# Kernel tuning notes

Hardware: AMD Instinct MI355X
Metric: run time of the kernel (lower is better)

Reference implementation:

```python
import jax, jax.numpy as jnp
import numpy as np

N_NODES = 50000
N_EDGES = 800000
FEATS = 128
HIDDEN = 64
CLASSES = 64


def graph_conv(x, edges):
    """GCN-style symmetric-normalized aggregation over an edge list (no self-loops;
    self information is supplied via the concat in the host module)."""
    src, dst = edges[0], edges[1]
    ones = jnp.ones((edges.shape[1],), dtype=x.dtype)
    deg = jax.ops.segment_sum(ones, dst, num_segments=N_NODES)
    inv_sqrt = jax.lax.rsqrt(jnp.maximum(deg, 1.0))
    coef = inv_sqrt[src] * inv_sqrt[dst]            # [E]
    msg = x[src] * coef[:, None]                     # [E, H] gather
    return jax.ops.segment_sum(msg, dst, num_segments=N_NODES)  # [N, H] scatter


def setup_inputs() -> dict:
    key = jax.random.key(0)
    ks = jax.random.split(key, 16)
    def lin(k, out_d, in_d):
        return jax.random.normal(k, (out_d, in_d), dtype=jnp.float32) / np.sqrt(in_d)
    x = jax.random.normal(ks[0], (N_NODES, FEATS), dtype=jnp.float32)
    edges = jax.random.randint(ks[1], (2, N_EDGES), 0, N_NODES, dtype=jnp.int64)
    return {
        "x": x,
        "edges": edges,
        "W1": lin(ks[2], HIDDEN, FEATS),
        "b1": jnp.zeros((HIDDEN,), dtype=jnp.float32),
        "W2": lin(ks[3], HIDDEN, 2 * HIDDEN),
        "A2a": lin(ks[4], HIDDEN, HIDDEN),
        "A2b": lin(ks[5], HIDDEN, HIDDEN),
        "W3": lin(ks[6], HIDDEN, 2 * HIDDEN),
        "A3a": lin(ks[7], HIDDEN, HIDDEN),
        "A3b": lin(ks[8], HIDDEN, HIDDEN),
        "W4": lin(ks[9], CLASSES, 2 * HIDDEN),
        "A4a": lin(ks[10], CLASSES, HIDDEN),
        "A4b": lin(ks[11], CLASSES, HIDDEN),
    }


def _block(x, edges, W, Aa, Ab):
    # relu(Linear(cat[x, conv(x)]) + att_a(x) * att_b(x))
    h = graph_conv(x, edges)
    cat = jnp.concatenate([x, h], axis=1)            # [N, 2H]
    return jax.nn.relu(cat @ W.T + (x @ Aa.T) * (x @ Ab.T))


def reference(x, edges, W1, b1, W2, A2a, A2b, W3, A3a, A3b, W4, A4a, A4b):
    x = jax.nn.relu(x @ W1.T + b1)                   # [N, H]
    x = _block(x, edges, W2, A2a, A2b)               # [N, H]
    x = _block(x, edges, W3, A3a, A3b)               # [N, H]
    x = _block(x, edges, W4, A4a, A4b)               # [N, C]
    return x
```

## Files before the change

kernel.cpp:

```cpp
#include <hip/hip_runtime.h>
#include <hip/hip_bf16.h>
#include <hip/hip_fp16.h>

#define N_NODES 50000
#define N_EDGES 800000
#define NTILES 3125
#define W_TOTAL 57344
#define WB2 192
#define TB 782
#define ROWCAP 64
#define ZROW N_NODES

#define NBKT 200
#define BKT_NODES 250
#define BKT_CAP 4400
#define ABLK 256
#define ACH ((N_EDGES + ABLK - 1) / ABLK)

typedef __attribute__((ext_vector_type(8))) short bf16x8;
typedef __attribute__((ext_vector_type(4))) float f32x4;
typedef __attribute__((ext_vector_type(2))) float f32x2;
typedef __attribute__((ext_vector_type(8))) unsigned short u16x8;
typedef __attribute__((ext_vector_type(4))) unsigned int u32x4;

__device__ inline unsigned short f2bf(float f) {
    unsigned int x = __float_as_uint(f);
    unsigned int r = (x + 0x7FFF + ((x >> 16) & 1)) >> 16;
    return (unsigned short)r;
}
__device__ inline float2 h2f2(unsigned int u) {
    __half2 h = *(__half2*)&u;
    return make_float2(__low2float(h), __high2float(h));
}
__device__ inline unsigned int f22h2(float a, float b) {
    __half2 h = __floats2half2_rn(a, b);
    return *(unsigned int*)&h;
}

__global__ __launch_bounds__(256) void passA_kernel(
    const float* __restrict__ x, const int* __restrict__ src, const int* __restrict__ dst,
    const float* __restrict__ W1, const float* __restrict__ b1,
    const float* W2, const float* A2a, const float* A2b,
    const float* W3, const float* A3a, const float* A3b,
    const float* W4, const float* A4a, const float* A4b,
    int* __restrict__ bucketCnt, unsigned int* __restrict__ bktArr,
    unsigned short* __restrict__ wp, __half* __restrict__ Ht,
    unsigned char* __restrict__ As8, unsigned char* __restrict__ Bs8) {
    int tid = threadIdx.x;

    if (blockIdx.x < ABLK) {
        __shared__ int hist[NBKT];
        __shared__ int gbase[NBKT];
        __shared__ int hoff[NBKT];
        if (tid < NBKT) { hist[tid] = 0; hoff[tid] = 0; }
        __syncthreads();
        int e0 = blockIdx.x * ACH;
        int e1 = min(e0 + ACH, N_EDGES);
        for (int e = e0 + tid; e < e1; e += 256)
            atomicAdd(&hist[dst[e] / BKT_NODES], 1);
        __syncthreads();
        if (tid < NBKT) {
            int h = hist[tid];
            gbase[tid] = h ? atomicAdd(&bucketCnt[tid], h) : 0;
        }
        __syncthreads();
        for (int e = e0 + tid; e < e1; e += 256) {
            int d = dst[e];
            int b = d / BKT_NODES;
            int pos = gbase[b] + atomicAdd(&hoff[b], 1);
            if (pos < BKT_CAP)
                bktArr[(size_t)b * BKT_CAP + pos] =
                    ((unsigned int)(d - b * BKT_NODES) << 16) | (unsigned int)src[e];
        }
        return;
    }
    if (blockIdx.x >= ABLK + TB) {
        if (blockIdx.x == ABLK + TB) {
            if (tid < 16)      ((unsigned int*)(As8 + (size_t)ZROW * 64))[tid] = 0u;
            else if (tid < 32) ((unsigned int*)(Bs8 + (size_t)ZROW * 64))[tid - 16] = 0u;
        }
        int i = 8192 + (blockIdx.x - ABLK - TB) * 256 + tid;
        if (i >= W_TOTAL) return;
        float v;
        if (i < 16384)      v = W2[i - 8192];
        else if (i < 20480) v = A2a[i - 16384];
        else if (i < 24576) v = A2b[i - 20480];
        else if (i < 32768) v = W3[i - 24576];
        else if (i < 36864) v = A3a[i - 32768];
        else if (i < 40960) v = A3b[i - 36864];
        else if (i < 49152) v = W4[i - 40960];
        else if (i < 53248) v = A4a[i - 49152];
        else                v = A4b[i - 53248];
        wp[i] = f2bf(v);
        return;
    }

    int wave = ((blockIdx.x - ABLK) * 256 + tid) >> 6;
    if (wave >= NTILES) return;
    int lane = tid & 63;
    int r16 = lane & 15, quad = lane >> 4;
    int base = wave * 16;

    bf16x8 a[4];
    const float* xr = x + (size_t)(base + r16) * 128 + quad * 8;
#pragma unroll
    for (int kb = 0; kb < 4; kb++) {
        float4 f0 = *(const float4*)(xr + kb * 32);
        float4 f1 = *(const float4*)(xr + kb * 32 + 4);
        bf16x8 v;
        v[0] = (short)f2bf(f0.x); v[1] = (short)f2bf(f0.y);
        v[2] = (short)f2bf(f0.z); v[3] = (short)f2bf(f0.w);
        v[4] = (short)f2bf(f1.x); v[5] = (short)f2bf(f1.y);
        v[6] = (short)f2bf(f1.z); v[7] = (short)f2bf(f1.w);
        a[kb] = v;
    }

#pragma unroll
    for (int jt = 0; jt < 4; jt++) {
        f32x4 acc = {0.f, 0.f, 0.f, 0.f};
        const float* wr = W1 + (size_t)(jt * 16 + r16) * 128 + quad * 8;
#pragma unroll
        for (int kb = 0; kb < 4; kb++) {
            float4 g0 = *(const float4*)(wr + kb * 32);
            float4 g1 = *(const float4*)(wr + kb * 32 + 4);
            bf16x8 b;
            b[0] = (short)f2bf(g0.x); b[1] = (short)f2bf(g0.y);
            b[2] = (short)f2bf(g0.z); b[3] = (short)f2bf(g0.w);
            b[4] = (short)f2bf(g1.x); b[5] = (short)f2bf(g1.y);
            b[6] = (short)f2bf(g1.z); b[7] = (short)f2bf(g1.w);
            acc = __builtin_amdgcn_mfma_f32_16x16x32_bf16(a[kb], b, acc, 0, 0, 0);
        }
        int col = jt * 16 + r16;
        float bias = b1[col];
#pragma unroll
        for (int r = 0; r < 4; r++) {
            int row = base + quad * 4 + r;
            float v = fmaxf(acc[r] + bias, 0.f);
            Ht[(size_t)row * 64 + col] = __float2half(v);
        }
    }
}

__global__ __launch_bounds__(256) void csr_scale_k(const int* __restrict__ bucketCnt,
                                                   const unsigned int* __restrict__ bktArr,
                                                   const __half* __restrict__ Ht,
                                                   unsigned short* __restrict__ srcAp,
                                                   int* __restrict__ cnt,
                                                   __half* __restrict__ As,
                                                   unsigned char* __restrict__ As8,
                                                   float* __restrict__ isq,
                                                   float* __restrict__ sdeg) {
    __shared__ int lcnt[BKT_NODES];
    int b = blockIdx.x, tid = threadIdx.x;
    if (tid < BKT_NODES) lcnt[tid] = 0;
    __syncthreads();
    int n = min(bucketCnt[b], BKT_CAP);
    int rowbase = b * BKT_NODES;
    const unsigned int* arr = bktArr + (size_t)b * BKT_CAP;
    for (int i = tid; i < n; i += 256) {
        unsigned int u = arr[i];
        int dl = (int)(u >> 16);
        int pos = atomicAdd(&lcnt[dl], 1);
        if (pos < ROWCAP)
            srcAp[(size_t)(rowbase + dl) * ROWCAP + pos] = (unsigned short)(u & 0xFFFF);
    }
    __syncthreads();
    if (tid < BKT_NODES) {
        int deg = lcnt[tid];
        int cv = min(deg, ROWCAP);
        int cvr = (cv + 7) & ~7;
        for (int j = cv; j < cvr; j++)
            srcAp[(size_t)(rowbase + tid) * ROWCAP + j] = (unsigned short)ZROW;
        cnt[rowbase + tid] = deg;
        float dv = fmaxf((float)deg, 1.0f);
        isq[rowbase + tid] = rsqrtf(dv);
        sdeg[rowbase + tid] = sqrtf(dv);
    }
    __syncthreads();
    int sl = tid & 15;
    for (int rr = tid >> 4; rr < BKT_NODES; rr += 16) {
        int row = rowbase + rr;
        float is = rsqrtf(fmaxf((float)lcnt[rr], 1.0f));
        uint2 rv = *((const uint2*)(Ht + (size_t)row * 64) + sl);
        float2 fa = h2f2(rv.x), fb = h2f2(rv.y);
        float s0 = fa.x * is, s1 = fa.y * is, s2 = fb.x * is, s3 = fb.y * is;
        uint2 ov;
        ov.x = f22h2(s0, s1);
        ov.y = f22h2(s2, s3);
        *((uint2*)(As + (size_t)row * 64) + sl) = ov;
        unsigned int w = __builtin_amdgcn_cvt_pk_fp8_f32(s0, s1, 0, false);
        w = __builtin_amdgcn_cvt_pk_fp8_f32(s2, s3, w, true);
        ((unsigned int*)As8)[(size_t)row * 16 + sl] = w;
    }
}

__global__ __launch_bounds__(256) void conv_dense_k(const __half* __restrict__ hs,
                                                    const unsigned char* __restrict__ hs8,
                                                    const int* __restrict__ cnt,
                                                    const unsigned short* __restrict__ srcAp,
                                                    const float* __restrict__ isq,
                                                    const float* __restrict__ sdeg,
                                                    const unsigned short* __restrict__ wp,
                                                    const unsigned short* __restrict__ aap,
                                                    const unsigned short* __restrict__ abp,
                                                    __half* __restrict__ outs,
                                                    unsigned char* __restrict__ outs8,
                                                    float* __restrict__ outf,
                                                    int finalLayer) {
    __shared__ unsigned short clds[64][64];
    int tid = threadIdx.x;
    int wv = tid >> 6;
    int lane = tid & 63;
    int t = blockIdx.x * 4 + wv;
    if (t >= NTILES) return;
    int base = t * 16;

    {
        int r = lane >> 2, fl = lane & 3;
        int row = base + r;
        int b = row * ROWCAP;
        int cv = min(cnt[row], ROWCAP);
        int cvr = (cv + 7) & ~7;
        f32x2 acc[8];
#pragma unroll
        for (int k = 0; k < 8; k++) acc[k] = (f32x2){0.f, 0.f};
        if (cvr) {
            u16x8 sv = __builtin_nontemporal_load((const u16x8*)(srcAp + b));
            for (int i = 0; i < cvr; i += 8) {
                u16x8 svn = sv;
                if (i + 8 < cvr)
                    svn = __builtin_nontemporal_load((const u16x8*)(srcAp + b + i + 8));
                u32x4 rv[8];
#pragma unroll
                for (int u = 0; u < 8; u++)
                    rv[u] = *((const u32x4*)(hs8 + (size_t)(int)sv[u] * 64) + fl);
#pragma unroll
                for (int u = 0; u < 8; u++) {
                    acc[0] += __builtin_amdgcn_cvt_pk_f32_fp8(rv[u][0], false);
                    acc[1] += __builtin_amdgcn_cvt_pk_f32_fp8(rv[u][0], true);
                    acc[2] += __builtin_amdgcn_cvt_pk_f32_fp8(rv[u][1], false);
                    acc[3] += __builtin_amdgcn_cvt_pk_f32_fp8(rv[u][1], true);
                    acc[4] += __builtin_amdgcn_cvt_pk_f32_fp8(rv[u][2], false);
                    acc[5] += __builtin_amdgcn_cvt_pk_f32_fp8(rv[u][2], true);
                    acc[6] += __builtin_amdgcn_cvt_pk_f32_fp8(rv[u][3], false);
                    acc[7] += __builtin_amdgcn_cvt_pk_f32_fp8(rv[u][3], true);
                }
                sv = svn;
            }
        }
        float sc = isq[row];
        u16x8 o0, o1;
#pragma unroll
        for (int k = 0; k < 4; k++) {
            o0[2 * k]     = f2bf(acc[k][0] * sc);
            o0[2 * k + 1] = f2bf(acc[k][1] * sc);
            o1[2 * k]     = f2bf(acc[4 + k][0] * sc);
            o1[2 * k + 1] = f2bf(acc[4 + k][1] * sc);
        }
        *(u16x8*)(&clds[wv * 16 + r][fl * 16]) = o0;
        *(u16x8*)(&clds[wv * 16 + r][fl * 16 + 8]) = o1;
    }

    int r16 = lane & 15, quad = lane >> 4;
    float rs = sdeg[base + r16];
    const u32x4* hp = (const u32x4*)(hs + (size_t)(base + r16) * 64);
    u32x4 raw0 = __builtin_nontemporal_load(hp + quad);
    u32x4 raw1 = __builtin_nontemporal_load(hp + 4 + quad);
    bf16x8 ha0, ha1;
    {
        float2 f;
        f = h2f2(raw0[0]); ha0[0] = (short)f2bf(f.x * rs); ha0[1] = (short)f2bf(f.y * rs);
        f = h2f2(raw0[1]); ha0[2] = (short)f2bf(f.x * rs); ha0[3] = (short)f2bf(f.y * rs);
        f = h2f2(raw0[2]); ha0[4] = (short)f2bf(f.x * rs); ha0[5] = (short)f2bf(f.y * rs);
        f = h2f2(raw0[3]); ha0[6] = (short)f2bf(f.x * rs); ha0[7] = (short)f2bf(f.y * rs);
        f = h2f2(raw1[0]); ha1[0] = (short)f2bf(f.x * rs); ha1[1] = (short)f2bf(f.y * rs);
        f = h2f2(raw1[1]); ha1[2] = (short)f2bf(f.x * rs); ha1[3] = (short)f2bf(f.y * rs);
        f = h2f2(raw1[2]); ha1[4] = (short)f2bf(f.x * rs); ha1[5] = (short)f2bf(f.y * rs);
        f = h2f2(raw1[3]); ha1[6] = (short)f2bf(f.x * rs); ha1[7] = (short)f2bf(f.y * rs);
    }
    bf16x8 ca0 = *(const bf16x8*)(&clds[wv * 16 + r16][quad * 8]);
    bf16x8 ca1 = *(const bf16x8*)(&clds[wv * 16 + r16][32 + quad * 8]);

    float isq4[4];
    if (!finalLayer) {
#pragma unroll
        for (int r = 0; r < 4; r++) isq4[r] = isq[base + quad * 4 + r];
    }

#pragma unroll
    for (int jt = 0; jt < 4; jt++) {
        const unsigned short* wr = wp + (size_t)(jt * 16 + r16) * 128 + quad * 8;
        const unsigned short* ar = aap + (size_t)(jt * 16 + r16) * 64 + quad * 8;
        const unsigned short* br = abp + (size_t)(jt * 16 + r16) * 64 + quad * 8;
        f32x4 P = {0.f, 0.f, 0.f, 0.f};
        f32x4 Q = {0.f, 0.f, 0.f, 0.f};
        f32x4 R = {0.f, 0.f, 0.f, 0.f};
        P = __builtin_amdgcn_mfma_f32_16x16x32_bf16(ha0, *(const bf16x8*)(wr), P, 0, 0, 0);
        P = __builtin_amdgcn_mfma_f32_16x16x32_bf16(ha1, *(const bf16x8*)(wr + 32), P, 0, 0, 0);
        P = __builtin_amdgcn_mfma_f32_16x16x32_bf16(ca0, *(const bf16x8*)(wr + 64), P, 0, 0, 0);
        P = __builtin_amdgcn_mfma_f32_16x16x32_bf16(ca1, *(const bf16x8*)(wr + 96), P, 0, 0, 0);
        Q = __builtin_amdgcn_mfma_f32_16x16x32_bf16(ha0, *(const bf16x8*)(ar), Q, 0, 0, 0);
        Q = __builtin_amdgcn_mfma_f32_16x16x32_bf16(ha1, *(const bf16x8*)(ar + 32), Q, 0, 0, 0);
        R = __builtin_amdgcn_mfma_f32_16x16x32_bf16(ha0, *(const bf16x8*)(br), R, 0, 0, 0);
        R = __builtin_amdgcn_mfma_f32_16x16x32_bf16(ha1, *(const bf16x8*)(br + 32), R, 0, 0, 0);
        int col = jt * 16 + r16;
#pragma unroll
        for (int r = 0; r < 4; r++) {
            int row = base + quad * 4 + r;
            float v = fmaxf(P[r] + Q[r] * R[r], 0.f);
            if (finalLayer) {
                __builtin_nontemporal_store(v, &outf[(size_t)row * 64 + col]);
            } else {
                float vs = v * isq4[r];
                __half hv = __float2half(vs);
                __builtin_nontemporal_store(*(unsigned short*)&hv,
                                            (unsigned short*)outs + (size_t)row * 64 + col);
                unsigned int pb = __builtin_amdgcn_cvt_pk_fp8_f32(vs, vs, 0, false);
                __builtin_nontemporal_store((unsigned char)pb,
                                            &outs8[(size_t)row * 64 + col]);
            }
        }
    }
}

extern "C" void kernel_launch(void* const* d_in, const int* in_sizes, int n_in,
                              void* d_out, int out_size, void* d_ws, size_t ws_size,
                              hipStream_t stream) {
    const float* x = (const float*)d_in[0];
    const int* edges = (const int*)d_in[1];
    const float* W1 = (const float*)d_in[2];
    const float* b1 = (const float*)d_in[3];
    const float* W2 = (const float*)d_in[4];
    const float* A2a = (const float*)d_in[5];
    const float* A2b = (const float*)d_in[6];
    const float* W3 = (const float*)d_in[7];
    const float* A3a = (const float*)d_in[8];
    const float* A3b = (const float*)d_in[9];
    const float* W4 = (const float*)d_in[10];
    const float* A4a = (const float*)d_in[11];
    const float* A4b = (const float*)d_in[12];
    float* out = (float*)d_out;

    const int* src = edges;
    const int* dst = edges + N_EDGES;

    char* p = (char*)d_ws;
    auto alloc = [&](size_t bytes) {
        char* r = p;
        p += (bytes + 255) & ~(size_t)255;
        return r;
    };
    int* bucketCnt        = (int*)alloc(NBKT * 4);
    unsigned int* bktArr  = (unsigned int*)alloc((size_t)NBKT * BKT_CAP * 4);
    int* cnt              = (int*)alloc(N_NODES * 4);
    float* isq            = (float*)alloc(N_NODES * 4);
    float* sdeg           = (float*)alloc(N_NODES * 4);
    unsigned short* srcAp = (unsigned short*)alloc((size_t)N_NODES * ROWCAP * 2);
    unsigned short* wpAll = (unsigned short*)alloc(W_TOTAL * 2);
    __half* Ht            = (__half*)alloc((size_t)N_NODES * 64 * 2);
    __half* As            = (__half*)alloc((size_t)N_NODES * 64 * 2);
    __half* Bs            = (__half*)alloc((size_t)N_NODES * 64 * 2);
    unsigned char* As8    = (unsigned char*)alloc((size_t)(N_NODES + 1) * 64);
    unsigned char* Bs8    = (unsigned char*)alloc((size_t)(N_NODES + 1) * 64);

    const unsigned short* W2p  = wpAll + 8192;
    const unsigned short* A2ap = wpAll + 16384;
    const unsigned short* A2bp = wpAll + 20480;
    const unsigned short* W3p  = wpAll + 24576;
    const unsigned short* A3ap = wpAll + 32768;
    const unsigned short* A3bp = wpAll + 36864;
    const unsigned short* W4p  = wpAll + 40960;
    const unsigned short* A4ap = wpAll + 49152;
    const unsigned short* A4bp = wpAll + 53248;

    hipMemsetAsync(bucketCnt, 0, NBKT * 4, stream);

    passA_kernel<<<ABLK + TB + WB2, 256, 0, stream>>>(
        x, src, dst, W1, b1, W2, A2a, A2b, W3, A3a, A3b, W4, A4a, A4b,
        bucketCnt, bktArr, wpAll, Ht, As8, Bs8);

    csr_scale_k<<<NBKT, 256, 0, stream>>>(bucketCnt, bktArr, Ht, srcAp, cnt,
                                          As, As8, isq, sdeg);

    conv_dense_k<<<TB, 256, 0, stream>>>(As, As8, cnt, srcAp, isq, sdeg,
                                         W2p, A2ap, A2bp, Bs, Bs8, nullptr, 0);
    conv_dense_k<<<TB, 256, 0, stream>>>(Bs, Bs8, cnt, srcAp, isq, sdeg,
                                         W3p, A3ap, A3bp, As, As8, nullptr, 0);
    conv_dense_k<<<TB, 256, 0, stream>>>(As, As8, cnt, srcAp, isq, sdeg,
                                         W4p, A4ap, A4bp, nullptr, nullptr, out, 1);
}
```

Measured before the change: 226.5 us.

## Spread gather-aggregation over 8 lanes per row and halve tiles per block

The conv kernel's neighbour gather now uses 8 threads per destination row, each loading 8 fp8 bytes, instead of 4 threads loading 16 bytes. Each 256-thread block covers 2 tiles (32 rows), and block count doubles. A __syncthreads separates the gather from the dense MFMA stage, which now runs on only 2 of the 4 waves. The aim is more memory-level parallelism and shorter per-thread dependency chains in the latency-bound gather. The cost is half the waves idling during the dense stage and an added block-wide barrier.

```diff
diff --git a/kernel.cpp b/kernel.cpp
--- a/kernel.cpp
+++ b/kernel.cpp
@@ -8,6 +8,7 @@
 #define W_TOTAL 57344
 #define WB2 192
 #define TB 782
+#define CB 1563
 #define ROWCAP 64
 #define ZROW N_NODES
 
@@ -207,60 +208,59 @@
                                                     unsigned char* __restrict__ outs8,
                                                     float* __restrict__ outf,
                                                     int finalLayer) {
-    __shared__ unsigned short clds[64][64];
+    __shared__ unsigned short clds[32][64];
     int tid = threadIdx.x;
+    int t0 = blockIdx.x * 2;
+    int rowbase = t0 * 16;
+
+    {
+        int lrow = tid >> 3, fl = tid & 7;
+        int row = rowbase + lrow;
+        if (row < N_NODES) {
+            int b = row * ROWCAP;
+            int cv = min(cnt[row], ROWCAP);
+            int cvr = (cv + 7) & ~7;
+            f32x2 acc[4];
+#pragma unroll
+            for (int k = 0; k < 4; k++) acc[k] = (f32x2){0.f, 0.f};
+            if (cvr) {
+                u16x8 sv = __builtin_nontemporal_load((const u16x8*)(srcAp + b));
+                for (int i = 0; i < cvr; i += 8) {
+                    u16x8 svn = sv;
+                    if (i + 8 < cvr)
+                        svn = __builtin_nontemporal_load((const u16x8*)(srcAp + b + i + 8));
+                    uint2 rv[8];
+#pragma unroll
+                    for (int u = 0; u < 8; u++)
+                        rv[u] = *((const uint2*)(hs8 + (size_t)(int)sv[u] * 64) + fl);
+#pragma unroll
+                    for (int u = 0; u < 8; u++) {
+                        acc[0] += __builtin_amdgcn_cvt_pk_f32_fp8(rv[u].x, false);
+                        acc[1] += __builtin_amdgcn_cvt_pk_f32_fp8(rv[u].x, true);
+                        acc[2] += __builtin_amdgcn_cvt_pk_f32_fp8(rv[u].y, false);
+                        acc[3] += __builtin_amdgcn_cvt_pk_f32_fp8(rv[u].y, true);
+                    }
+                    sv = svn;
+                }
+            }
+            float sc = isq[row];
+            u16x8 o;
+#pragma unroll
+            for (int k = 0; k < 4; k++) {
+                o[2 * k]     = f2bf(acc[k][0] * sc);
+                o[2 * k + 1] = f2bf(acc[k][1] * sc);
+            }
+            *(u16x8*)(&clds[lrow][fl * 8]) = o;
+        }
+    }
+    __syncthreads();
+
     int wv = tid >> 6;
-    int lane = tid & 63;
-    int t = blockIdx.x * 4 + wv;
+    if (wv >= 2) return;
+    int t = t0 + wv;
     if (t >= NTILES) return;
     int base = t * 16;
-
-    {
-        int r = lane >> 2, fl = lane & 3;
-        int row = base + r;
-        int b = row * ROWCAP;
-        int cv = min(cnt[row], ROWCAP);
-        int cvr = (cv + 7) & ~7;
-        f32x2 acc[8];
-#pragma unroll
-        for (int k = 0; k < 8; k++) acc[k] = (f32x2){0.f, 0.f};
-        if (cvr) {
-            u16x8 sv = __builtin_nontemporal_load((const u16x8*)(srcAp + b));
-            for (int i = 0; i < cvr; i += 8) {
-                u16x8 svn = sv;
-                if (i + 8 < cvr)
-                    svn = __builtin_nontemporal_load((const u16x8*)(srcAp + b + i + 8));
-                u32x4 rv[8];
-#pragma unroll
-                for (int u = 0; u < 8; u++)
-                    rv[u] = *((const u32x4*)(hs8 + (size_t)(int)sv[u] * 64) + fl);
-#pragma unroll
-                for (int u = 0; u < 8; u++) {
-                    acc[0] += __builtin_amdgcn_cvt_pk_f32_fp8(rv[u][0], false);
-                    acc[1] += __builtin_amdgcn_cvt_pk_f32_fp8(rv[u][0], true);
-                    acc[2] += __builtin_amdgcn_cvt_pk_f32_fp8(rv[u][1], false);
-                    acc[3] += __builtin_amdgcn_cvt_pk_f32_fp8(rv[u][1], true);
-                    acc[4] += __builtin_amdgcn_cvt_pk_f32_fp8(rv[u][2], false);
-                    acc[5] += __builtin_amdgcn_cvt_pk_f32_fp8(rv[u][2], true);
-                    acc[6] += __builtin_amdgcn_cvt_pk_f32_fp8(rv[u][3], false);
-                    acc[7] += __builtin_amdgcn_cvt_pk_f32_fp8(rv[u][3], true);
-                }
-                sv = svn;
-            }
-        }
-        float sc = isq[row];
-        u16x8 o0, o1;
-#pragma unroll
-        for (int k = 0; k < 4; k++) {
-            o0[2 * k]     = f2bf(acc[k][0] * sc);
-            o0[2 * k + 1] = f2bf(acc[k][1] * sc);
-            o1[2 * k]     = f2bf(acc[4 + k][0] * sc);
-            o1[2 * k + 1] = f2bf(acc[4 + k][1] * sc);
-        }
-        *(u16x8*)(&clds[wv * 16 + r][fl * 16]) = o0;
-        *(u16x8*)(&clds[wv * 16 + r][fl * 16 + 8]) = o1;
-    }
-
+    int lane = tid & 63;
     int r16 = lane & 15, quad = lane >> 4;
     float rs = sdeg[base + r16];
     const u32x4* hp = (const u32x4*)(hs + (size_t)(base + r16) * 64);
@@ -382,10 +382,10 @@
     csr_scale_k<<<NBKT, 256, 0, stream>>>(bucketCnt, bktArr, Ht, srcAp, cnt,
                                           As, As8, isq, sdeg);
 
-    conv_dense_k<<<TB, 256, 0, stream>>>(As, As8, cnt, srcAp, isq, sdeg,
+    conv_dense_k<<<CB, 256, 0, stream>>>(As, As8, cnt, srcAp, isq, sdeg,
                                          W2p, A2ap, A2bp, Bs, Bs8, nullptr, 0);
-    conv_dense_k<<<TB, 256, 0, stream>>>(Bs, Bs8, cnt, srcAp, isq, sdeg,
+    conv_dense_k<<<CB, 256, 0, stream>>>(Bs, Bs8, cnt, srcAp, isq, sdeg,
                                          W3p, A3ap, A3bp, As, As8, nullptr, 0);
-    conv_dense_k<<<TB, 256, 0, stream>>>(As, As8, cnt, srcAp, isq, sdeg,
+    conv_dense_k<<<CB, 256, 0, stream>>>(As, As8, cnt, srcAp, isq, sdeg,
                                          W4p, A4ap, A4bp, nullptr, nullptr, out, 1);
 }
```

After: 223.9 us. No clear change (-1.1%).
